# Optimization experiments

Hardware: AMD Instinct MI355X
Metric: run time of the kernel (lower is better)

The kernel has to match this reference:

```python
import jax, jax.numpy as jnp
import numpy as np

BITS = 8
BOUND = 2.0 ** (BITS - 1) - 1.0  # 127, symmetric int8 bound
EPS = 1e-6


def fake_quant(x, scale):
    """Symmetric fake quantization with straight-through estimator."""
    q = jnp.clip(jnp.round(x * scale), -BOUND, BOUND) / scale
    return x + jax.lax.stop_gradient(q - x)


def dense_aqt(x, w, b, mask):
    """AQT-style quantized dense: per-tensor input scale (masked stats),
    per-output-channel weight scale, int8-range fake quant, float GEMM.
    x: [N, Cin], w: [Cin, Cout], b: [Cout], mask: [N, 1]."""
    x_max = jnp.max(jnp.abs(x * mask))                       # masked per-tensor stat
    sx = BOUND / jnp.maximum(x_max, EPS)
    w_max = jnp.max(jnp.abs(w), axis=0, keepdims=True)        # [1, Cout]
    sw = BOUND / jnp.maximum(w_max, EPS)
    xq = fake_quant(x, sx)
    wq = fake_quant(w, sw)
    return jnp.matmul(xq, wq) + b


def setup_inputs() -> dict:
    key = jax.random.key(0)
    k1, k2, k3 = jax.random.split(key, 3)
    B, S, C, H = 4, 2048, 1024, 4096
    inputs = jax.random.normal(k1, (B, S, C), dtype=jnp.float32)
    padding_mask = jnp.ones((B, S, 1), dtype=jnp.float32)
    W1 = jax.random.normal(k2, (C, H), dtype=jnp.float32) * (1.0 / np.sqrt(C))
    b1 = jnp.zeros((H,), dtype=jnp.float32)
    W2 = jax.random.normal(k3, (H, C), dtype=jnp.float32) * (1.0 / np.sqrt(H))
    b2 = jnp.zeros((C,), dtype=jnp.float32)
    return {"inputs": inputs, "padding_mask": padding_mask,
            "W1": W1, "b1": b1, "W2": W2, "b2": b2}


def reference(inputs, padding_mask, W1, b1, W2, b2):
    B, S, C = inputs.shape
    x = inputs.reshape(B * S, C)
    m = padding_mask.reshape(B * S, 1)
    h = jax.nn.relu(dense_aqt(x, W1, b1, m))   # dropout is no-op (deterministic)
    out = dense_aqt(h, W2, b2, m)              # dropout is no-op (deterministic)
    return out.reshape(B, S, C)
```

## Files before the change

kernel.cpp:

```cpp
#include <hip/hip_runtime.h>
#include <hip/hip_fp16.h>
#include <stdint.h>


#define EPSQ 1e-6f
typedef int v4i __attribute__((ext_vector_type(4)));
typedef int v16i __attribute__((ext_vector_type(16)));

__device__ __forceinline__ void async16(const int8_t* g, int8_t* l) {
  __builtin_amdgcn_global_load_lds(
      (const __attribute__((address_space(1))) void*)g,
      (__attribute__((address_space(3))) void*)l, 16, 0, 0);
}
__device__ __forceinline__ unsigned short f2h(float f) {
  __half h = __float2half(f);
  return *(unsigned short*)&h;
}
__device__ __forceinline__ float4 max4(float4 m, float4 v) {
  m.x = fmaxf(m.x, fabsf(v.x)); m.y = fmaxf(m.y, fabsf(v.y));
  m.z = fmaxf(m.z, fabsf(v.z)); m.w = fmaxf(m.w, fabsf(v.w));
  return m;
}
__device__ __forceinline__ unsigned qmb(float x, float s) {
  return __float_as_uint(fmaf(x, s, 12582912.0f)) & 0xffu;
}
__device__ __forceinline__ unsigned q4f(float4 f, float s) {
  return qmb(f.x, s) | (qmb(f.y, s) << 8) | (qmb(f.z, s) << 16) |
         (__float_as_uint(fmaf(f.w, s, 12582912.0f)) << 24);
}
__device__ __forceinline__ unsigned q4h(unsigned ua, unsigned ub,
                                        __half2 s2, __half2 m2) {
  __half2 ha = __hfma2(*(__half2*)&ua, s2, m2);
  __half2 hb = __hfma2(*(__half2*)&ub, s2, m2);
  unsigned va = *(unsigned*)&ha, vb = *(unsigned*)&hb;
#if __has_builtin(__builtin_amdgcn_perm)
  return __builtin_amdgcn_perm(vb, va, 0x06040200u);
#else
  return (va & 0xffu) | ((va >> 8) & 0xff00u) |
         ((vb & 0xffu) << 16) | (((vb >> 8) & 0xff00u) << 16);
#endif
}

__global__ __launch_bounds__(256) void k_stats(
    const float* __restrict__ x, const float* __restrict__ mask,
    const float* __restrict__ W1, const float* __restrict__ W2,
    float* __restrict__ pmaxX, float* __restrict__ pcm1, float* __restrict__ pcm2) {
  const int bx = blockIdx.x, tid = threadIdx.x;
  if (bx < 64) {
    const int sp = bx & 15, cg = bx >> 4;
    const int col = cg * 1024 + tid * 4;
    float4 m = {0.f, 0.f, 0.f, 0.f};
#pragma unroll 8
    for (int r = 0; r < 64; ++r)
      m = max4(m, *(const float4*)(W1 + (size_t)(sp * 64 + r) * 4096 + col));
    *(float4*)(pcm1 + sp * 4096 + col) = m;
  } else if (bx < 128) {
    const int sp = bx - 64;
    const int col = tid * 4;
    float4 m = {0.f, 0.f, 0.f, 0.f};
#pragma unroll 8
    for (int r = 0; r < 64; ++r)
      m = max4(m, *(const float4*)(W2 + (size_t)(sp * 64 + r) * 1024 + col));
    *(float4*)(pcm2 + sp * 1024 + col) = m;
  } else {
    __shared__ float red[4];
    const int b = bx - 128;
    float lmax = 0.f;
    for (int c = b * 256 + tid; c < 1048576; c += 262144) {
      size_t idx = (size_t)c * 8;
      float mk = fabsf(mask[idx >> 10]);
      float4 m4 = {0.f, 0.f, 0.f, 0.f};
      m4 = max4(m4, *(const float4*)(x + idx));
      m4 = max4(m4, *(const float4*)(x + idx + 4));
      lmax = fmaxf(lmax, fmaxf(fmaxf(m4.x, m4.y), fmaxf(m4.z, m4.w)) * mk);
    }
    for (int s = 32; s; s >>= 1) lmax = fmaxf(lmax, __shfl_down(lmax, s));
    if ((tid & 63) == 0) red[tid >> 6] = lmax;
    __syncthreads();
    if (tid == 0)
      pmaxX[b] = fmaxf(fmaxf(red[0], red[1]), fmaxf(red[2], red[3]));
  }
}

__global__ __launch_bounds__(256) void k_quant(
    const float* __restrict__ x, const float* __restrict__ W1, const float* __restrict__ W2,
    const float* __restrict__ pmaxX, const float* __restrict__ pcm1, const float* __restrict__ pcm2,
    int8_t* __restrict__ qx, int8_t* __restrict__ qw1, int8_t* __restrict__ qw2,
    float* __restrict__ cm1, float* __restrict__ cm2, float* __restrict__ scG) {
  const int bx = blockIdx.x, tid = threadIdx.x;
  if (bx < 2048) {
    __shared__ float red[4];
    float v = fmaxf(fmaxf(pmaxX[tid], pmaxX[tid + 256]),
                    fmaxf(pmaxX[tid + 512], pmaxX[tid + 768]));
    for (int s = 32; s; s >>= 1) v = fmaxf(v, __shfl_down(v, s));
    if ((tid & 63) == 0) red[tid >> 6] = v;
    __syncthreads();
    const float xmax = fmaxf(fmaxf(red[0], red[1]), fmaxf(red[2], red[3]));
    if (bx == 0 && tid == 0) scG[0] = xmax;
    const float s = 127.0f / fmaxf(xmax, EPSQ);
    const int wave = tid >> 6, lane = tid & 63;
    const int f = bx * 4 + wave;
    const int r = (f >> 5) * 32 + (lane & 31);
    const int k = (f & 31) * 32 + (lane >> 5) * 16;
    const float4* src = (const float4*)(x + (size_t)r * 1024 + k);
    uint4 o;
    o.x = q4f(src[0], s); o.y = q4f(src[1], s);
    o.z = q4f(src[2], s); o.w = q4f(src[3], s);
    *(uint4*)(qx + (size_t)f * 1024 + lane * 16) = o;
  } else if (bx < 2304) {
    int id = (bx - 2048) * 256 + tid;
    int n4 = id & 1023, kc = id >> 10;
    const int col = n4 * 4;
    float4 cm = {0.f, 0.f, 0.f, 0.f};
#pragma unroll
    for (int sp = 0; sp < 16; ++sp) {
      float4 p = *(const float4*)(pcm1 + sp * 4096 + col);
      cm.x = fmaxf(cm.x, p.x); cm.y = fmaxf(cm.y, p.y);
      cm.z = fmaxf(cm.z, p.z); cm.w = fmaxf(cm.w, p.w);
    }
    if (kc == 0) *(float4*)(cm1 + col) = cm;
    const float s0 = 127.0f / fmaxf(cm.x, EPSQ), s1 = 127.0f / fmaxf(cm.y, EPSQ);
    const float s2 = 127.0f / fmaxf(cm.z, EPSQ), s3 = 127.0f / fmaxf(cm.w, EPSQ);
    union { int8_t p[16]; uint4 v; } u0, u1, u2, u3;
#pragma unroll
    for (int j = 0; j < 16; ++j) {
      float4 f = *(const float4*)(W1 + (size_t)(kc * 16 + j) * 4096 + col);
      u0.p[j] = (int8_t)qmb(f.x, s0); u1.p[j] = (int8_t)qmb(f.y, s1);
      u2.p[j] = (int8_t)qmb(f.z, s2); u3.p[j] = (int8_t)qmb(f.w, s3);
    }
    int8_t* base = qw1 + ((size_t)(col >> 5) * 32 + (kc >> 1)) * 1024 +
                   (kc & 1) * 512 + (col & 31) * 16;
    *(uint4*)(base) = u0.v;      *(uint4*)(base + 16) = u1.v;
    *(uint4*)(base + 32) = u2.v; *(uint4*)(base + 48) = u3.v;
  } else {
    int id = (bx - 2304) * 256 + tid;
    int n4 = id & 255, kc = id >> 8;
    const int col = n4 * 4;
    float4 cm = {0.f, 0.f, 0.f, 0.f};
#pragma unroll
    for (int sp = 0; sp < 64; ++sp) {
      float4 p = *(const float4*)(pcm2 + sp * 1024 + col);
      cm.x = fmaxf(cm.x, p.x); cm.y = fmaxf(cm.y, p.y);
      cm.z = fmaxf(cm.z, p.z); cm.w = fmaxf(cm.w, p.w);
    }
    if (kc == 0) *(float4*)(cm2 + col) = cm;
    const float s0 = 127.0f / fmaxf(cm.x, EPSQ), s1 = 127.0f / fmaxf(cm.y, EPSQ);
    const float s2 = 127.0f / fmaxf(cm.z, EPSQ), s3 = 127.0f / fmaxf(cm.w, EPSQ);
    union { int8_t p[16]; uint4 v; } u0, u1, u2, u3;
#pragma unroll
    for (int j = 0; j < 16; ++j) {
      float4 f = *(const float4*)(W2 + (size_t)(kc * 16 + j) * 1024 + col);
      u0.p[j] = (int8_t)qmb(f.x, s0); u1.p[j] = (int8_t)qmb(f.y, s1);
      u2.p[j] = (int8_t)qmb(f.z, s2); u3.p[j] = (int8_t)qmb(f.w, s3);
    }
    int8_t* base = qw2 + ((size_t)(col >> 5) * 128 + (kc >> 1)) * 1024 +
                   (kc & 1) * 512 + (col & 31) * 16;
    *(uint4*)(base) = u0.v;      *(uint4*)(base + 16) = u1.v;
    *(uint4*)(base + 32) = u2.v; *(uint4*)(base + 48) = u3.v;
  }
}

__global__ __launch_bounds__(512, 4) void gemm1(
    const int8_t* __restrict__ A, const int8_t* __restrict__ Bt,
    const float* __restrict__ sxp, const float* __restrict__ cmax,
    const float* __restrict__ bias, const float* __restrict__ mask,
    unsigned short* __restrict__ hfrag, float* __restrict__ pmaxH) {
  constexpr int NST = 16;
  __shared__ __align__(16) int8_t smem[2 * 8192];
  const int tid = threadIdx.x;
  const int wave = tid >> 6, lane = tid & 63;

  const int bid = blockIdx.x;
  const int xcd = bid & 7, sl = bid >> 3;
  const int m0 = (xcd * 4 + (sl & 3)) * 256;
  const int n0 = (sl >> 2) * 128;
  const int wr = wave & 3, wc = wave >> 2;

  v16i acc[2][2] = {};

  const int8_t* gA = A + ((size_t)((m0 >> 5) + wr * 2) * 32) * 1024 + lane * 16;
  const int kcS = wave >> 2, nbS = wave & 3;
  const int8_t* gB = Bt + ((size_t)((n0 >> 5) + nbS) * 32 + kcS) * 1024 + lane * 16;
  const int dBo = wave * 1024 + lane * 16;
  const int rdo = wc * 2048 + lane * 16;

  v4i aP0, aP1, aP2, aP3, aQ0, aQ1, aQ2, aQ3;

  async16(gB, smem + dBo);
  __builtin_amdgcn_sched_barrier(0);
  aP0 = *(const v4i*)(gA);
  aP1 = *(const v4i*)(gA + 1024);
  aP2 = *(const v4i*)(gA + 32768);
  aP3 = *(const v4i*)(gA + 32768 + 1024);
  asm volatile("s_waitcnt vmcnt(4)" ::: "memory");
  __builtin_amdgcn_s_barrier();
  __builtin_amdgcn_sched_barrier(0);

#pragma unroll 2
  for (int kb = 0; kb < NST; ++kb) {
    const int slot = (kb & 1) * 8192, nslot = slot ^ 8192;
    const bool more = (kb + 1 < NST);
    if (more) {
      async16(gB + (size_t)(kb + 1) * 2048, smem + nslot + dBo);
      __builtin_amdgcn_sched_barrier(0);
      const int8_t* ga = gA + (size_t)(kb + 1) * 2048;
      if (kb & 1) {
        aP0 = *(const v4i*)(ga);         aP1 = *(const v4i*)(ga + 1024);
        aP2 = *(const v4i*)(ga + 32768); aP3 = *(const v4i*)(ga + 32768 + 1024);
      } else {
        aQ0 = *(const v4i*)(ga);         aQ1 = *(const v4i*)(ga + 1024);
        aQ2 = *(const v4i*)(ga + 32768); aQ3 = *(const v4i*)(ga + 32768 + 1024);
      }
      __builtin_amdgcn_sched_barrier(0);
    }
    {
      const v4i a00 = (kb & 1) ? aQ0 : aP0;
      const v4i a01 = (kb & 1) ? aQ1 : aP1;
      const v4i a10 = (kb & 1) ? aQ2 : aP2;
      const v4i a11 = (kb & 1) ? aQ3 : aP3;
      v4i b0 = *(const v4i*)(smem + slot + rdo);
      v4i b1 = *(const v4i*)(smem + slot + rdo + 1024);
      __builtin_amdgcn_s_setprio(1);
      acc[0][0] = __builtin_amdgcn_mfma_i32_32x32x32_i8(a00, b0, acc[0][0], 0, 0, 0);
      acc[0][1] = __builtin_amdgcn_mfma_i32_32x32x32_i8(a00, b1, acc[0][1], 0, 0, 0);
      acc[1][0] = __builtin_amdgcn_mfma_i32_32x32x32_i8(a10, b0, acc[1][0], 0, 0, 0);
      acc[1][1] = __builtin_amdgcn_mfma_i32_32x32x32_i8(a10, b1, acc[1][1], 0, 0, 0);
      __builtin_amdgcn_s_setprio(0);
      v4i b2 = *(const v4i*)(smem + slot + 4096 + rdo);
      v4i b3 = *(const v4i*)(smem + slot + 4096 + rdo + 1024);
      __builtin_amdgcn_s_setprio(1);
      acc[0][0] = __builtin_amdgcn_mfma_i32_32x32x32_i8(a01, b2, acc[0][0], 0, 0, 0);
      acc[0][1] = __builtin_amdgcn_mfma_i32_32x32x32_i8(a01, b3, acc[0][1], 0, 0, 0);
      acc[1][0] = __builtin_amdgcn_mfma_i32_32x32x32_i8(a11, b2, acc[1][0], 0, 0, 0);
      acc[1][1] = __builtin_amdgcn_mfma_i32_32x32x32_i8(a11, b3, acc[1][1], 0, 0, 0);
      __builtin_amdgcn_s_setprio(0);
    }
    if (more) {
      asm volatile("s_waitcnt vmcnt(4)" ::: "memory");
      __builtin_amdgcn_s_barrier();
      __builtin_amdgcn_sched_barrier(0);
    }
  }

  const float asc = fmaxf(sxp[0], EPSQ) * (1.0f / 127.0f);
  const int cl = lane & 31;
  const int rbase = 4 * (lane >> 5);
  float bsc[2], bv[2];
#pragma unroll
  for (int nt = 0; nt < 2; ++nt) {
    const int col = n0 + wc * 64 + nt * 32 + cl;
    bsc[nt] = fmaxf(cmax[col], EPSQ) * (1.0f / 127.0f) * asc;
    bv[nt] = bias[col];
  }
  const int hwoff = (cl >> 4) * 512 + (cl & 15);
  float lmax = 0.f;
#pragma unroll
  for (int mt = 0; mt < 2; ++mt) {
    const int rowbase = m0 + wr * 64 + mt * 32;
    const size_t rowblk = (size_t)(rowbase >> 5);
#pragma unroll
    for (int g = 0; g < 4; ++g)
#pragma unroll
      for (int r2 = 0; r2 < 4; ++r2) {
        const int rloc = g * 8 + r2 + rbase;
        const float mk = fabsf(mask[rowbase + rloc]);
#pragma unroll
        for (int nt = 0; nt < 2; ++nt) {
          const size_t kblk = (size_t)((n0 + wc * 64 + nt * 32) >> 5);
          float v = (float)acc[mt][nt][g * 4 + r2] * bsc[nt] + bv[nt];
          v = fmaxf(v, 0.f);
          hfrag[(rowblk * 128 + kblk) * 1024 + hwoff + rloc * 16] = f2h(v);
          lmax = fmaxf(lmax, v * mk);
        }
      }
  }
  for (int s = 32; s; s >>= 1) lmax = fmaxf(lmax, __shfl_down(lmax, s));
  __syncthreads();
  float* redf = (float*)smem;
  if (lane == 0) redf[wave] = lmax;
  __syncthreads();
  if (tid == 0) {
    float r = redf[0];
#pragma unroll
    for (int j = 1; j < 8; ++j) r = fmaxf(r, redf[j]);
    pmaxH[bid] = r;
  }
}

__global__ __launch_bounds__(256, 3) void gemm2(
    const unsigned short* __restrict__ hfrag, const int8_t* __restrict__ Bt,
    const float* __restrict__ pmaxH, const float* __restrict__ cmax,
    const float* __restrict__ bias, float* __restrict__ out) {
  constexpr int NST = 64;
  __shared__ __align__(16) int8_t smem[2 * 8192];
  const int tid = threadIdx.x;
  const int wave = tid >> 6, lane = tid & 63;

  float* red = (float*)smem;
  float v = 0.f;
#pragma unroll
  for (int j = 0; j < 4; ++j) v = fmaxf(v, pmaxH[tid + 256 * j]);
  for (int s = 32; s; s >>= 1) v = fmaxf(v, __shfl_down(v, s));
  if (lane == 0) red[wave] = v;
  __syncthreads();
  const float hmax = fmaxf(fmaxf(red[0], red[1]), fmaxf(red[2], red[3]));
  __syncthreads();
  const float asc = fmaxf(hmax, EPSQ) * (1.0f / 127.0f);
  const __half sh = __float2half_rn(127.0f / fmaxf(hmax, EPSQ));
  const __half2 s2 = __halves2half2(sh, sh);
  const __half mh = __float2half_rn(1536.0f);
  const __half2 m2 = __halves2half2(mh, mh);

  const int bid = blockIdx.x;
  const int xcd = bid & 7, slot2 = bid >> 3;
  const int m0 = ((xcd << 3) + (slot2 >> 3)) * 128;
  const int n0 = (slot2 & 7) * 128;

  v16i acc[4] = {};

  const uint4* hA = (const uint4*)hfrag;
  const size_t aBase = ((size_t)((m0 >> 5) + wave) * 128) * 128 + (size_t)lane * 2;
  const int8_t* gB = Bt + ((size_t)((n0 >> 5) + wave) * 128) * 1024 + lane * 16;
  const int dB0o = wave * 1024 + lane * 16;
  const int dB1o = (4 + wave) * 1024 + lane * 16;
  const int rdo = lane * 16;

  uint4 hP0, hP1, hP2, hP3, hQ0, hQ1, hQ2, hQ3;

  async16(gB, smem + dB0o);
  async16(gB + 1024, smem + dB1o);
  __builtin_amdgcn_sched_barrier(0);
  hP0 = hA[aBase];       hP1 = hA[aBase + 1];
  hP2 = hA[aBase + 128]; hP3 = hA[aBase + 129];
  asm volatile("s_waitcnt vmcnt(4)" ::: "memory");
  __builtin_amdgcn_s_barrier();
  __builtin_amdgcn_sched_barrier(0);

#pragma unroll 2
  for (int kb = 0; kb < NST; ++kb) {
    const int slot = (kb & 1) * 8192, nslot = slot ^ 8192;
    const bool more = (kb + 1 < NST);
    if (more) {
      async16(gB + (size_t)((kb + 1) * 2) * 1024,     smem + nslot + dB0o);
      async16(gB + (size_t)((kb + 1) * 2 + 1) * 1024, smem + nslot + dB1o);
      __builtin_amdgcn_sched_barrier(0);
      const size_t ai = aBase + (size_t)((kb + 1) * 2) * 128;
      if (kb & 1) {
        hP0 = hA[ai];       hP1 = hA[ai + 1];
        hP2 = hA[ai + 128]; hP3 = hA[ai + 129];
      } else {
        hQ0 = hA[ai];       hQ1 = hA[ai + 1];
        hQ2 = hA[ai + 128]; hQ3 = hA[ai + 129];
      }
      __builtin_amdgcn_sched_barrier(0);
    }
    {
      const uint4 h0 = (kb & 1) ? hQ0 : hP0;
      const uint4 h1 = (kb & 1) ? hQ1 : hP1;
      const uint4 h2 = (kb & 1) ? hQ2 : hP2;
      const uint4 h3 = (kb & 1) ? hQ3 : hP3;
      uint4 oa, ob;
      oa.x = q4h(h0.x, h0.y, s2, m2); oa.y = q4h(h0.z, h0.w, s2, m2);
      oa.z = q4h(h1.x, h1.y, s2, m2); oa.w = q4h(h1.z, h1.w, s2, m2);
      ob.x = q4h(h2.x, h2.y, s2, m2); ob.y = q4h(h2.z, h2.w, s2, m2);
      ob.z = q4h(h3.x, h3.y, s2, m2); ob.w = q4h(h3.z, h3.w, s2, m2);
      const v4i af0 = *(const v4i*)&oa;
      const v4i af1 = *(const v4i*)&ob;
      v4i b0 = *(const v4i*)(smem + slot + rdo);
      v4i b1 = *(const v4i*)(smem + slot + 1024 + rdo);
      v4i b2 = *(const v4i*)(smem + slot + 2048 + rdo);
      v4i b3 = *(const v4i*)(smem + slot + 3072 + rdo);
      __builtin_amdgcn_s_setprio(1);
      acc[0] = __builtin_amdgcn_mfma_i32_32x32x32_i8(af0, b0, acc[0], 0, 0, 0);
      acc[1] = __builtin_amdgcn_mfma_i32_32x32x32_i8(af0, b1, acc[1], 0, 0, 0);
      acc[2] = __builtin_amdgcn_mfma_i32_32x32x32_i8(af0, b2, acc[2], 0, 0, 0);
      acc[3] = __builtin_amdgcn_mfma_i32_32x32x32_i8(af0, b3, acc[3], 0, 0, 0);
      __builtin_amdgcn_s_setprio(0);
      b0 = *(const v4i*)(smem + slot + 4096 + rdo);
      b1 = *(const v4i*)(smem + slot + 5120 + rdo);
      b2 = *(const v4i*)(smem + slot + 6144 + rdo);
      b3 = *(const v4i*)(smem + slot + 7168 + rdo);
      __builtin_amdgcn_s_setprio(1);
      acc[0] = __builtin_amdgcn_mfma_i32_32x32x32_i8(af1, b0, acc[0], 0, 0, 0);
      acc[1] = __builtin_amdgcn_mfma_i32_32x32x32_i8(af1, b1, acc[1], 0, 0, 0);
      acc[2] = __builtin_amdgcn_mfma_i32_32x32x32_i8(af1, b2, acc[2], 0, 0, 0);
      acc[3] = __builtin_amdgcn_mfma_i32_32x32x32_i8(af1, b3, acc[3], 0, 0, 0);
      __builtin_amdgcn_s_setprio(0);
    }
    if (more) {
      asm volatile("s_waitcnt vmcnt(4)" ::: "memory");
      __builtin_amdgcn_s_barrier();
      __builtin_amdgcn_sched_barrier(0);
    }
  }

  const int cl = lane & 31;
  const int rbase = 4 * (lane >> 5);
  float bsc[4], bv[4];
  int colv[4];
#pragma unroll
  for (int nf = 0; nf < 4; ++nf) {
    colv[nf] = n0 + nf * 32 + cl;
    bsc[nf] = fmaxf(cmax[colv[nf]], EPSQ) * (1.0f / 127.0f) * asc;
    bv[nf] = bias[colv[nf]];
  }
#pragma unroll
  for (int g = 0; g < 4; ++g)
#pragma unroll
    for (int r2 = 0; r2 < 4; ++r2) {
      const int row = m0 + wave * 32 + g * 8 + r2 + rbase;
#pragma unroll
      for (int nf = 0; nf < 4; ++nf)
        out[(size_t)row * 1024 + colv[nf]] =
            (float)acc[nf][g * 4 + r2] * bsc[nf] + bv[nf];
    }
}

extern "C" void kernel_launch(void* const* d_in, const int* in_sizes, int n_in,
                              void* d_out, int out_size, void* d_ws, size_t ws_size,
                              hipStream_t stream) {
  const float* x  = (const float*)d_in[0];
  const float* mk = (const float*)d_in[1];
  const float* W1 = (const float*)d_in[2];
  const float* b1 = (const float*)d_in[3];
  const float* W2 = (const float*)d_in[4];
  const float* b2 = (const float*)d_in[5];
  float* out = (float*)d_out;

  float* scG   = (float*)d_ws;
  float* pmaxX = scG + 8;
  float* pmaxH = pmaxX + 1024;
  float* pcm1  = pmaxH + 2048;
  float* pcm2  = pcm1 + 65536;
  float* cm1   = pcm2 + 65536;
  float* cm2   = cm1 + 4096;
  int8_t* qx  = (int8_t*)(cm2 + 1024);
  int8_t* qw1 = qx  + (size_t)8192 * 1024;
  int8_t* qw2 = qw1 + (size_t)4096 * 1024;
  unsigned short* h = (unsigned short*)(qw2 + (size_t)1024 * 4096);

  k_stats<<<1152, 256, 0, stream>>>(x, mk, W1, W2, pmaxX, pcm1, pcm2);
  k_quant<<<2560, 256, 0, stream>>>(x, W1, W2, pmaxX, pcm1, pcm2,
                                    qx, qw1, qw2, cm1, cm2, scG);
  gemm1<<<1024, 512, 0, stream>>>(qx, qw1, scG, cm1, b1, mk, h, pmaxH);
  gemm2<<<512, 256, 0, stream>>>(h, qw2, pmaxH, cm2, b2, out);
}
```

Before: 225.4 us.

## Deepen both int8 GEMMs to 4-stage LDS pipelines and retile to 128x128

```diff
diff --git a/kernel.cpp b/kernel.cpp
--- a/kernel.cpp
+++ b/kernel.cpp
@@ -166,80 +166,74 @@
     const float* __restrict__ bias, const float* __restrict__ mask,
     unsigned short* __restrict__ hfrag, float* __restrict__ pmaxH) {
   constexpr int NST = 16;
-  __shared__ __align__(16) int8_t smem[2 * 8192];
+  __shared__ __align__(16) int8_t smem[4 * 8192];
   const int tid = threadIdx.x;
   const int wave = tid >> 6, lane = tid & 63;
 
   const int bid = blockIdx.x;
   const int xcd = bid & 7, sl = bid >> 3;
-  const int m0 = (xcd * 4 + (sl & 3)) * 256;
-  const int n0 = (sl >> 2) * 128;
+  const int m0 = (xcd * 8 + (sl & 7)) * 128;
+  const int n0 = (sl >> 3) * 128;
   const int wr = wave & 3, wc = wave >> 2;
 
-  v16i acc[2][2] = {};
-
-  const int8_t* gA = A + ((size_t)((m0 >> 5) + wr * 2) * 32) * 1024 + lane * 16;
-  const int kcS = wave >> 2, nbS = wave & 3;
-  const int8_t* gB = Bt + ((size_t)((n0 >> 5) + nbS) * 32 + kcS) * 1024 + lane * 16;
+  v16i acc[2] = {};
+
+  const int8_t* gA = A + ((size_t)((m0 >> 5) + wr) * 32) * 1024 + lane * 16;
+  const int8_t* gB = Bt + ((size_t)((n0 >> 5) + (wave & 3)) * 32 + (wave >> 2)) * 1024
+                     + lane * 16;
   const int dBo = wave * 1024 + lane * 16;
-  const int rdo = wc * 2048 + lane * 16;
-
-  v4i aP0, aP1, aP2, aP3, aQ0, aQ1, aQ2, aQ3;
-
-  async16(gB, smem + dBo);
+  const int rdo = lane * 16;
+
+  v4i a0k0 = {}, a0k1 = {}, a1k0 = {}, a1k1 = {};
+  v4i a2k0 = {}, a2k1 = {}, a3k0 = {}, a3k1 = {};
+
+  async16(gB,        smem + dBo);
+  async16(gB + 2048, smem + 8192 + dBo);
+  async16(gB + 4096, smem + 16384 + dBo);
   __builtin_amdgcn_sched_barrier(0);
-  aP0 = *(const v4i*)(gA);
-  aP1 = *(const v4i*)(gA + 1024);
-  aP2 = *(const v4i*)(gA + 32768);
-  aP3 = *(const v4i*)(gA + 32768 + 1024);
-  asm volatile("s_waitcnt vmcnt(4)" ::: "memory");
+  a0k0 = *(const v4i*)(gA);        a0k1 = *(const v4i*)(gA + 1024);
+  a1k0 = *(const v4i*)(gA + 2048); a1k1 = *(const v4i*)(gA + 3072);
+  a2k0 = *(const v4i*)(gA + 4096); a2k1 = *(const v4i*)(gA + 5120);
+  asm volatile("s_waitcnt vmcnt(8)" ::: "memory");
   __builtin_amdgcn_s_barrier();
   __builtin_amdgcn_sched_barrier(0);
 
-#pragma unroll 2
+#pragma unroll 4
   for (int kb = 0; kb < NST; ++kb) {
-    const int slot = (kb & 1) * 8192, nslot = slot ^ 8192;
-    const bool more = (kb + 1 < NST);
-    if (more) {
-      async16(gB + (size_t)(kb + 1) * 2048, smem + nslot + dBo);
+    const int slot = (kb & 3) * 8192;
+    if (kb + 3 < NST) {
+      async16(gB + (size_t)(kb + 3) * 2048, smem + ((kb + 3) & 3) * 8192 + dBo);
       __builtin_amdgcn_sched_barrier(0);
-      const int8_t* ga = gA + (size_t)(kb + 1) * 2048;
-      if (kb & 1) {
-        aP0 = *(const v4i*)(ga);         aP1 = *(const v4i*)(ga + 1024);
-        aP2 = *(const v4i*)(ga + 32768); aP3 = *(const v4i*)(ga + 32768 + 1024);
-      } else {
-        aQ0 = *(const v4i*)(ga);         aQ1 = *(const v4i*)(ga + 1024);
-        aQ2 = *(const v4i*)(ga + 32768); aQ3 = *(const v4i*)(ga + 32768 + 1024);
-      }
+      const int8_t* ga = gA + (size_t)(kb + 3) * 2048;
+      const int d = (kb + 3) & 3;
+      if (d == 0)      { a0k0 = *(const v4i*)ga; a0k1 = *(const v4i*)(ga + 1024); }
+      else if (d == 1) { a1k0 = *(const v4i*)ga; a1k1 = *(const v4i*)(ga + 1024); }
+      else if (d == 2) { a2k0 = *(const v4i*)ga; a2k1 = *(const v4i*)(ga + 1024); }
+      else             { a3k0 = *(const v4i*)ga; a3k1 = *(const v4i*)(ga + 1024); }
       __builtin_amdgcn_sched_barrier(0);
     }
     {
-      const v4i a00 = (kb & 1) ? aQ0 : aP0;
-      const v4i a01 = (kb & 1) ? aQ1 : aP1;
-      const v4i a10 = (kb & 1) ? aQ2 : aP2;
-      const v4i a11 = (kb & 1) ? aQ3 : aP3;
-      v4i b0 = *(const v4i*)(smem + slot + rdo);
-      v4i b1 = *(const v4i*)(smem + slot + rdo + 1024);
+      const int s = kb & 3;
+      v4i af0, af1;
+      if (s == 0)      { af0 = a0k0; af1 = a0k1; }
+      else if (s == 1) { af0 = a1k0; af1 = a1k1; }
+      else if (s == 2) { af0 = a2k0; af1 = a2k1; }
+      else             { af0 = a3k0; af1 = a3k1; }
+      v4i b00 = *(const v4i*)(smem + slot + (0 * 4 + wc * 2 + 0) * 1024 + rdo);
+      v4i b01 = *(const v4i*)(smem + slot + (0 * 4 + wc * 2 + 1) * 1024 + rdo);
+      v4i b10 = *(const v4i*)(smem + slot + (1 * 4 + wc * 2 + 0) * 1024 + rdo);
+      v4i b11 = *(const v4i*)(smem + slot + (1 * 4 + wc * 2 + 1) * 1024 + rdo);
       __builtin_amdgcn_s_setprio(1);
-      acc[0][0] = __builtin_amdgcn_mfma_i32_32x32x32_i8(a00, b0, acc[0][0], 0, 0, 0);
-      acc[0][1] = __builtin_amdgcn_mfma_i32_32x32x32_i8(a00, b1, acc[0][1], 0, 0, 0);
-      acc[1][0] = __builtin_amdgcn_mfma_i32_32x32x32_i8(a10, b0, acc[1][0], 0, 0, 0);
-      acc[1][1] = __builtin_amdgcn_mfma_i32_32x32x32_i8(a10, b1, acc[1][1], 0, 0, 0);
+      acc[0] = __builtin_amdgcn_mfma_i32_32x32x32_i8(af0, b00, acc[0], 0, 0, 0);
+      acc[1] = __builtin_amdgcn_mfma_i32_32x32x32_i8(af0, b01, acc[1], 0, 0, 0);
+      acc[0] = __builtin_amdgcn_mfma_i32_32x32x32_i8(af1, b10, acc[0], 0, 0, 0);
+      acc[1] = __builtin_amdgcn_mfma_i32_32x32x32_i8(af1, b11, acc[1], 0, 0, 0);
       __builtin_amdgcn_s_setprio(0);
-      v4i b2 = *(const v4i*)(smem + slot + 4096 + rdo);
-      v4i b3 = *(const v4i*)(smem + slot + 4096 + rdo + 1024);
-      __builtin_amdgcn_s_setprio(1);
-      acc[0][0] = __builtin_amdgcn_mfma_i32_32x32x32_i8(a01, b2, acc[0][0], 0, 0, 0);
-      acc[0][1] = __builtin_amdgcn_mfma_i32_32x32x32_i8(a01, b3, acc[0][1], 0, 0, 0);
-      acc[1][0] = __builtin_amdgcn_mfma_i32_32x32x32_i8(a11, b2, acc[1][0], 0, 0, 0);
-      acc[1][1] = __builtin_amdgcn_mfma_i32_32x32x32_i8(a11, b3, acc[1][1], 0, 0, 0);
-      __builtin_amdgcn_s_setprio(0);
-    }
-    if (more) {
-      asm volatile("s_waitcnt vmcnt(4)" ::: "memory");
-      __builtin_amdgcn_s_barrier();
-      __builtin_amdgcn_sched_barrier(0);
-    }
+    }
+    if (kb + 3 < NST) asm volatile("s_waitcnt vmcnt(8)" ::: "memory");
+    else              asm volatile("s_waitcnt vmcnt(0)" ::: "memory");
+    __builtin_amdgcn_s_barrier();
+    __builtin_amdgcn_sched_barrier(0);
   }
 
   const float asc = fmaxf(sxp[0], EPSQ) * (1.0f / 127.0f);
@@ -253,27 +247,24 @@
     bv[nt] = bias[col];
   }
   const int hwoff = (cl >> 4) * 512 + (cl & 15);
+  const int rowbase = m0 + wr * 32;
+  const size_t rowblk = (size_t)(rowbase >> 5);
   float lmax = 0.f;
 #pragma unroll
-  for (int mt = 0; mt < 2; ++mt) {
-    const int rowbase = m0 + wr * 64 + mt * 32;
-    const size_t rowblk = (size_t)(rowbase >> 5);
-#pragma unroll
-    for (int g = 0; g < 4; ++g)
-#pragma unroll
-      for (int r2 = 0; r2 < 4; ++r2) {
-        const int rloc = g * 8 + r2 + rbase;
-        const float mk = fabsf(mask[rowbase + rloc]);
-#pragma unroll
-        for (int nt = 0; nt < 2; ++nt) {
-          const size_t kblk = (size_t)((n0 + wc * 64 + nt * 32) >> 5);
-          float v = (float)acc[mt][nt][g * 4 + r2] * bsc[nt] + bv[nt];
-          v = fmaxf(v, 0.f);
-          hfrag[(rowblk * 128 + kblk) * 1024 + hwoff + rloc * 16] = f2h(v);
-          lmax = fmaxf(lmax, v * mk);
-        }
+  for (int g = 0; g < 4; ++g)
+#pragma unroll
+    for (int r2 = 0; r2 < 4; ++r2) {
+      const int rloc = g * 8 + r2 + rbase;
+      const float mk = fabsf(mask[rowbase + rloc]);
+#pragma unroll
+      for (int nt = 0; nt < 2; ++nt) {
+        const size_t kblk = (size_t)((n0 + wc * 64 + nt * 32) >> 5);
+        float v = (float)acc[nt][g * 4 + r2] * bsc[nt] + bv[nt];
+        v = fmaxf(v, 0.f);
+        hfrag[(rowblk * 128 + kblk) * 1024 + hwoff + rloc * 16] = f2h(v);
+        lmax = fmaxf(lmax, v * mk);
       }
-  }
+    }
   for (int s = 32; s; s >>= 1) lmax = fmaxf(lmax, __shfl_down(lmax, s));
   __syncthreads();
   float* redf = (float*)smem;
@@ -287,23 +278,25 @@
   }
 }
 
-__global__ __launch_bounds__(256, 3) void gemm2(
+__global__ __launch_bounds__(512, 4) void gemm2(
     const unsigned short* __restrict__ hfrag, const int8_t* __restrict__ Bt,
     const float* __restrict__ pmaxH, const float* __restrict__ cmax,
     const float* __restrict__ bias, float* __restrict__ out) {
   constexpr int NST = 64;
-  __shared__ __align__(16) int8_t smem[2 * 8192];
+  __shared__ __align__(16) int8_t smem[4 * 8192];
   const int tid = threadIdx.x;
   const int wave = tid >> 6, lane = tid & 63;
 
   float* red = (float*)smem;
   float v = 0.f;
 #pragma unroll
-  for (int j = 0; j < 4; ++j) v = fmaxf(v, pmaxH[tid + 256 * j]);
+  for (int j = 0; j < 4; ++j) v = fmaxf(v, pmaxH[tid + 512 * j]);
   for (int s = 32; s; s >>= 1) v = fmaxf(v, __shfl_down(v, s));
   if (lane == 0) red[wave] = v;
   __syncthreads();
-  const float hmax = fmaxf(fmaxf(red[0], red[1]), fmaxf(red[2], red[3]));
+  float hmax = red[0];
+#pragma unroll
+  for (int j = 1; j < 8; ++j) hmax = fmaxf(hmax, red[j]);
   __syncthreads();
   const float asc = fmaxf(hmax, EPSQ) * (1.0f / 127.0f);
   const __half sh = __float2half_rn(127.0f / fmaxf(hmax, EPSQ));
@@ -315,45 +308,36 @@
   const int xcd = bid & 7, slot2 = bid >> 3;
   const int m0 = ((xcd << 3) + (slot2 >> 3)) * 128;
   const int n0 = (slot2 & 7) * 128;
-
-  v16i acc[4] = {};
+  const int wr = wave & 3, wc = wave >> 2;
+
+  v16i acc[2] = {};
 
   const uint4* hA = (const uint4*)hfrag;
-  const size_t aBase = ((size_t)((m0 >> 5) + wave) * 128) * 128 + (size_t)lane * 2;
-  const int8_t* gB = Bt + ((size_t)((n0 >> 5) + wave) * 128) * 1024 + lane * 16;
-  const int dB0o = wave * 1024 + lane * 16;
-  const int dB1o = (4 + wave) * 1024 + lane * 16;
+  const size_t aBase = ((size_t)((m0 >> 5) + wr) * 128) * 128 + (size_t)lane * 2;
+  const int8_t* gB = Bt + ((size_t)((n0 >> 5) + (wave & 3)) * 128 + (wave >> 2)) * 1024
+                     + lane * 16;
+  const int dBo = wave * 1024 + lane * 16;
   const int rdo = lane * 16;
 
-  uint4 hP0, hP1, hP2, hP3, hQ0, hQ1, hQ2, hQ3;
-
-  async16(gB, smem + dB0o);
-  async16(gB + 1024, smem + dB1o);
+  uint4 hP0 = {}, hP1 = {}, hP2 = {}, hP3 = {};
+  uint4 hQ0 = {}, hQ1 = {}, hQ2 = {}, hQ3 = {};
+
+  async16(gB,        smem + dBo);
+  async16(gB + 2048, smem + 8192 + dBo);
+  async16(gB + 4096, smem + 16384 + dBo);
   __builtin_amdgcn_sched_barrier(0);
   hP0 = hA[aBase];       hP1 = hA[aBase + 1];
   hP2 = hA[aBase + 128]; hP3 = hA[aBase + 129];
-  asm volatile("s_waitcnt vmcnt(4)" ::: "memory");
+  hQ0 = hA[aBase + 256]; hQ1 = hA[aBase + 257];
+  hQ2 = hA[aBase + 384]; hQ3 = hA[aBase + 385];
+  asm volatile("s_waitcnt vmcnt(10)" ::: "memory");
   __builtin_amdgcn_s_barrier();
   __builtin_amdgcn_sched_barrier(0);
 
-#pragma unroll 2
+#pragma unroll 4
   for (int kb = 0; kb < NST; ++kb) {
-    const int slot = (kb & 1) * 8192, nslot = slot ^ 8192;
-    const bool more = (kb + 1 < NST);
-    if (more) {
-      async16(gB + (size_t)((kb + 1) * 2) * 1024,     smem + nslot + dB0o);
-      async16(gB + (size_t)((kb + 1) * 2 + 1) * 1024, smem + nslot + dB1o);
-      __builtin_amdgcn_sched_barrier(0);
-      const size_t ai = aBase + (size_t)((kb + 1) * 2) * 128;
-      if (kb & 1) {
-        hP0 = hA[ai];       hP1 = hA[ai + 1];
-        hP2 = hA[ai + 128]; hP3 = hA[ai + 129];
-      } else {
-        hQ0 = hA[ai];       hQ1 = hA[ai + 1];
-        hQ2 = hA[ai + 128]; hQ3 = hA[ai + 129];
-      }
-      __builtin_amdgcn_sched_barrier(0);
-    }
+    const int slot = (kb & 3) * 8192;
+    v4i af0, af1;
     {
       const uint4 h0 = (kb & 1) ? hQ0 : hP0;
       const uint4 h1 = (kb & 1) ? hQ1 : hP1;
@@ -364,55 +348,57 @@
       oa.z = q4h(h1.x, h1.y, s2, m2); oa.w = q4h(h1.z, h1.w, s2, m2);
       ob.x = q4h(h2.x, h2.y, s2, m2); ob.y = q4h(h2.z, h2.w, s2, m2);
       ob.z = q4h(h3.x, h3.y, s2, m2); ob.w = q4h(h3.z, h3.w, s2, m2);
-      const v4i af0 = *(const v4i*)&oa;
-      const v4i af1 = *(const v4i*)&ob;
-      v4i b0 = *(const v4i*)(smem + slot + rdo);
-      v4i b1 = *(const v4i*)(smem + slot + 1024 + rdo);
-      v4i b2 = *(const v4i*)(smem + slot + 2048 + rdo);
-      v4i b3 = *(const v4i*)(smem + slot + 3072 + rdo);
+      af0 = *(const v4i*)&oa;
+      af1 = *(const v4i*)&ob;
+    }
+    __builtin_amdgcn_sched_barrier(0);
+    if (kb + 3 < NST)
+      async16(gB + (size_t)(kb + 3) * 2048, smem + ((kb + 3) & 3) * 8192 + dBo);
+    __builtin_amdgcn_sched_barrier(0);
+    if (kb + 2 < NST) {
+      const size_t ai = aBase + (size_t)(kb + 2) * 256;
+      if (kb & 1) { hQ0 = hA[ai]; hQ1 = hA[ai + 1]; hQ2 = hA[ai + 128]; hQ3 = hA[ai + 129]; }
+      else        { hP0 = hA[ai]; hP1 = hA[ai + 1]; hP2 = hA[ai + 128]; hP3 = hA[ai + 129]; }
+    }
+    __builtin_amdgcn_sched_barrier(0);
+    {
+      v4i b00 = *(const v4i*)(smem + slot + (0 * 4 + wc * 2 + 0) * 1024 + rdo);
+      v4i b01 = *(const v4i*)(smem + slot + (0 * 4 + wc * 2 + 1) * 1024 + rdo);
+      v4i b10 = *(const v4i*)(smem + slot + (1 * 4 + wc * 2 + 0) * 1024 + rdo);
+      v4i b11 = *(const v4i*)(smem + slot + (1 * 4 + wc * 2 + 1) * 1024 + rdo);
       __builtin_amdgcn_s_setprio(1);
-      acc[0] = __builtin_amdgcn_mfma_i32_32x32x32_i8(af0, b0, acc[0], 0, 0, 0);
-      acc[1] = __builtin_amdgcn_mfma_i32_32x32x32_i8(af0, b1, acc[1], 0, 0, 0);
-      acc[2] = __builtin_amdgcn_mfma_i32_32x32x32_i8(af0, b2, acc[2], 0, 0, 0);
-      acc[3] = __builtin_amdgcn_mfma_i32_32x32x32_i8(af0, b3, acc[3], 0, 0, 0);
+      acc[0] = __builtin_amdgcn_mfma_i32_32x32x32_i8(af0, b00, acc[0], 0, 0, 0);
+      acc[1] = __builtin_amdgcn_mfma_i32_32x32x32_i8(af0, b01, acc[1], 0, 0, 0);
+      acc[0] = __builtin_amdgcn_mfma_i32_32x32x32_i8(af1, b10, acc[0], 0, 0, 0);
+      acc[1] = __builtin_amdgcn_mfma_i32_32x32x32_i8(af1, b11, acc[1], 0, 0, 0);
       __builtin_amdgcn_s_setprio(0);
-      b0 = *(const v4i*)(smem + slot + 4096 + rdo);
-      b1 = *(const v4i*)(smem + slot + 5120 + rdo);
-      b2 = *(const v4i*)(smem + slot + 6144 + rdo);
-      b3 = *(const v4i*)(smem + slot + 7168 + rdo);
-      __builtin_amdgcn_s_setprio(1);
-      acc[0] = __builtin_amdgcn_mfma_i32_32x32x32_i8(af1, b0, acc[0], 0, 0, 0);
-      acc[1] = __builtin_amdgcn_mfma_i32_32x32x32_i8(af1, b1, acc[1], 0, 0, 0);
-      acc[2] = __builtin_amdgcn_mfma_i32_32x32x32_i8(af1, b2, acc[2], 0, 0, 0);
-      acc[3] = __builtin_amdgcn_mfma_i32_32x32x32_i8(af1, b3, acc[3], 0, 0, 0);
-      __builtin_amdgcn_s_setprio(0);
-    }
-    if (more) {
-      asm volatile("s_waitcnt vmcnt(4)" ::: "memory");
-      __builtin_amdgcn_s_barrier();
-      __builtin_amdgcn_sched_barrier(0);
-    }
+    }
+    if (kb + 3 < NST) asm volatile("s_waitcnt vmcnt(10)" ::: "memory");
+    else              asm volatile("s_waitcnt vmcnt(0)" ::: "memory");
+    __builtin_amdgcn_s_barrier();
+    __builtin_amdgcn_sched_barrier(0);
   }
 
   const int cl = lane & 31;
   const int rbase = 4 * (lane >> 5);
-  float bsc[4], bv[4];
-  int colv[4];
-#pragma unroll
-  for (int nf = 0; nf < 4; ++nf) {
-    colv[nf] = n0 + nf * 32 + cl;
-    bsc[nf] = fmaxf(cmax[colv[nf]], EPSQ) * (1.0f / 127.0f) * asc;
-    bv[nf] = bias[colv[nf]];
-  }
+  float bsc[2], bv[2];
+  int colv[2];
+#pragma unroll
+  for (int nt = 0; nt < 2; ++nt) {
+    colv[nt] = n0 + wc * 64 + nt * 32 + cl;
+    bsc[nt] = fmaxf(cmax[colv[nt]], EPSQ) * (1.0f / 127.0f) * asc;
+    bv[nt] = bias[colv[nt]];
+  }
+  const int rowbase = m0 + wr * 32;
 #pragma unroll
   for (int g = 0; g < 4; ++g)
 #pragma unroll
     for (int r2 = 0; r2 < 4; ++r2) {
-      const int row = m0 + wave * 32 + g * 8 + r2 + rbase;
-#pragma unroll
-      for (int nf = 0; nf < 4; ++nf)
-        out[(size_t)row * 1024 + colv[nf]] =
-            (float)acc[nf][g * 4 + r2] * bsc[nf] + bv[nf];
+      const int row = rowbase + g * 8 + r2 + rbase;
+#pragma unroll
+      for (int nt = 0; nt < 2; ++nt)
+        out[(size_t)row * 1024 + colv[nt]] =
+            (float)acc[nt][g * 4 + r2] * bsc[nt] + bv[nt];
     }
 }
 
@@ -442,6 +428,6 @@
   k_stats<<<1152, 256, 0, stream>>>(x, mk, W1, W2, pmaxX, pcm1, pcm2);
   k_quant<<<2560, 256, 0, stream>>>(x, W1, W2, pmaxX, pcm1, pcm2,
                                     qx, qw1, qw2, cm1, cm2, scG);
-  gemm1<<<1024, 512, 0, stream>>>(qx, qw1, scG, cm1, b1, mk, h, pmaxH);
-  gemm2<<<512, 256, 0, stream>>>(h, qw2, pmaxH, cm2, b2, out);
-}
+  gemm1<<<2048, 512, 0, stream>>>(qx, qw1, scG, cm1, b1, mk, h, pmaxH);
+  gemm2<<<512, 512, 0, stream>>>(h, qw2, pmaxH, cm2, b2, out);
+}
```

New measurement: 243.3 us. 1.08x slower.
